# Kernel tuning notes

Measured on AMD Instinct MI355X. Metric: run time of the kernel, lower is better.

The kernel has to match this reference:

```python
import jax, jax.numpy as jnp
import numpy as np

B, S, D, L, H = 2, 2048, 2048, 3, 16
DH = D // H
BLOCK = 16
NA = 64
Q = NA * BLOCK
KV = S + Q
VOCAB = 32000
MASK_ID = 31999
GAMMA = 7.0
EPS = 1e-6


def _rope(x, pos):
    # x: [B,H,T,DH], pos: [B,T]
    half = DH // 2
    inv = 1.0 / (10000.0 ** (jnp.arange(half, dtype=jnp.float32) / half))
    ang = pos[:, None, :, None].astype(jnp.float32) * inv  # [B,1,T,half]
    c, s = jnp.cos(ang), jnp.sin(ang)
    x1, x2 = x[..., :half], x[..., half:]
    return jnp.concatenate([x1 * c - x2 * s, x2 * c + x1 * s], axis=-1)


def setup_inputs() -> dict:
    key = jax.random.key(0)
    ks = jax.random.split(key, 12)
    w = lambda k, shp: 0.02 * jax.random.normal(k, shp, jnp.float32)
    return {
        'input_ids': jax.random.randint(ks[0], (B, S), 0, VOCAB, dtype=jnp.int32),
        'hidden_states': jax.random.normal(ks[1], (L, B, S, D), jnp.float32),
        'loss_mask': jnp.ones((B, S), jnp.int32),
        'lm_head_weight': w(ks[2], (VOCAB, D)),
        'norm_weight': jnp.ones((D,), jnp.float32),
        'anchor_positions': jnp.sort(jax.random.randint(ks[3], (B, NA), 0, S - BLOCK, dtype=jnp.int32), axis=-1),
        'ctx_proj_w': w(ks[4], (D, L * D)),
        'embed_table': w(ks[5], (VOCAB, D)),
        'wq': w(ks[6], (D, D)),
        'wk': w(ks[7], (D, D)),
        'wv': w(ks[8], (D, D)),
        'wo': w(ks[9], (D, D)),
    }


def reference(input_ids, hidden_states, loss_mask, lm_head_weight, norm_weight,
              anchor_positions, ctx_proj_w, embed_table, wq, wk, wv, wo):
    # --- context feature: concat L target-layer hiddens, project to D ---
    ctx_cat = jnp.transpose(hidden_states, (1, 2, 0, 3)).reshape(B, S, L * D)
    ctx = jnp.einsum('bsf,df->bsd', ctx_cat, ctx_proj_w)

    # --- position ids (context: 0..S-1; draft block i starts at anchor_i) ---
    ctx_pos = jnp.broadcast_to(jnp.arange(S, dtype=jnp.int32), (B, S))
    draft_pos = (anchor_positions[:, :, None] + jnp.arange(BLOCK, dtype=jnp.int32)[None, None, :]).reshape(B, Q)

    # --- draft input (anchor token + MASKs) and labels ---
    off = jnp.arange(Q, dtype=jnp.int32) % BLOCK                       # [Q]
    anchor_per_tok = jnp.repeat(anchor_positions, BLOCK, axis=1)       # [B,Q]
    anchor_tok = jnp.take_along_axis(input_ids, anchor_positions, axis=1)
    draft_ids = jnp.where(off[None, :] == 0, jnp.repeat(anchor_tok, BLOCK, axis=1), MASK_ID)
    labels = jnp.where(off[None, :] == 0, -100,
                       jnp.take_along_axis(input_ids, anchor_per_tok + off[None, :], axis=1))

    # --- block-causal mask: [B,Q,KV] ---
    qi = jnp.arange(Q, dtype=jnp.int32)
    ki = jnp.arange(KV, dtype=jnp.int32)
    qb = qi // BLOCK                                                   # [Q]
    apos = anchor_positions[:, qb]                                     # [B,Q]
    ctx_vis = (ki[None, None, :] < S) & (ki[None, None, :] < apos[:, :, None])
    kb = (ki - S) // BLOCK
    draft_vis = (ki >= S)[None, :] & (qb[:, None] == kb[None, :])      # [Q,KV]
    mask = ctx_vis | draft_vis[None]                                   # [B,Q,KV]

    # --- single RoPE attention layer: draft queries over [context; draft] ---
    emb = embed_table[draft_ids]                                       # [B,Q,D]
    x_kv = jnp.concatenate([ctx, emb], axis=1)                         # [B,KV,D]
    pos_kv = jnp.concatenate([ctx_pos, draft_pos], axis=1)             # [B,KV]
    q = _rope((emb @ wq.T).reshape(B, Q, H, DH).transpose(0, 2, 1, 3), draft_pos)
    k = _rope((x_kv @ wk.T).reshape(B, KV, H, DH).transpose(0, 2, 1, 3), pos_kv)
    v = (x_kv @ wv.T).reshape(B, KV, H, DH).transpose(0, 2, 1, 3)
    scores = jnp.einsum('bhqd,bhkd->bhqk', q, k) / np.float32(np.sqrt(DH))
    scores = jnp.where(mask[:, None], scores, jnp.float32(-1e30))
    attn = jax.nn.softmax(scores, axis=-1)
    out = jnp.einsum('bhqk,bhkd->bhqd', attn, v).transpose(0, 2, 1, 3).reshape(B, Q, D) @ wo.T
    hidden = emb + out

    # --- RMSNorm + LM head ---
    hidden = hidden * jax.lax.rsqrt(jnp.mean(hidden * hidden, -1, keepdims=True) + EPS) * norm_weight
    logits = hidden @ lm_head_weight.T                                 # [B,Q,VOCAB]

    # --- decay-weighted CE loss + accuracy ---
    logp = jax.nn.log_softmax(logits, axis=-1)
    lab = jnp.where(labels < 0, 0, labels)
    nll = -jnp.take_along_axis(logp, lab[..., None], axis=-1)[..., 0]
    valid = labels != -100
    offf = off.astype(jnp.float32)
    decay = jnp.where(off == 0, 0.0, jnp.exp(-(offf - 1.0) / GAMMA))   # [Q]
    w = decay[None, :] * valid.astype(jnp.float32)
    loss = jnp.sum(nll * w) / jnp.maximum(jnp.sum(w), 1e-6)
    preds = jnp.argmax(logits, axis=-1).astype(labels.dtype)
    acc = jnp.sum((preds == labels) & valid) / jnp.maximum(jnp.sum(valid), 1)
    return loss, acc.astype(jnp.float32)
```

## Files before the change

kernel.cpp:

```cpp
#include <hip/hip_runtime.h>

#define B_ 2
#define S_ 2048
#define D_ 2048
#define L_ 3
#define H_ 16
#define DH_ 128
#define BLK_ 16
#define NA_ 64
#define Q_ 1024
#define KV_ 3072
#define VOCAB_ 32000
#define MASK_ID_ 31999
#define NTOK_ (B_*Q_)
#define VT2_ (VOCAB_/256)
#define NCHUNK_ 4

typedef __attribute__((ext_vector_type(8))) short bf16x8;
typedef __attribute__((ext_vector_type(4))) float f32x4;
typedef const __attribute__((address_space(1))) void* gptr_t;
typedef __attribute__((address_space(3))) void* lptr_t;

__device__ inline unsigned short f2bf(float x) {
  unsigned int u = __float_as_uint(x);
  unsigned int r = (u + 0x7fff + ((u >> 16) & 1)) >> 16;
  return (unsigned short)r;
}
__device__ inline float bf2f(unsigned short u) {
  return __uint_as_float(((unsigned int)u) << 16);
}

__global__ void k_meta(const int* __restrict__ ids, const int* __restrict__ anchors,
                       int* __restrict__ dids, int* __restrict__ dpos, int* __restrict__ labels) {
  int t = blockIdx.x * 256 + threadIdx.x;
  if (t >= NTOK_) return;
  int b = t >> 10, qi = t & 1023;
  int a = qi >> 4, off = qi & 15;
  int ap = anchors[b * NA_ + a];
  dpos[t] = ap + off;
  dids[t] = (off == 0) ? ids[b * S_ + ap] : MASK_ID_;
  labels[t] = (off == 0) ? -100 : ids[b * S_ + ap + off];
}

__global__ void k_cvt(const float* __restrict__ in, unsigned short* __restrict__ out, int n4) {
  int i = blockIdx.x * 256 + threadIdx.x;
  if (i >= n4) return;
  float4 v = ((const float4*)in)[i];
  ushort4 o;
  o.x = f2bf(v.x); o.y = f2bf(v.y); o.z = f2bf(v.z); o.w = f2bf(v.w);
  ((ushort4*)out)[i] = o;
}

__global__ void k_cvt_ctx(const float* __restrict__ hs, unsigned short* __restrict__ out) {
  int bi = blockIdx.x;
  int l = bi % 3, row = bi / 3;
  const float4* src = (const float4*)(hs + ((size_t)l * B_ * S_ + row) * (size_t)D_);
  ushort4* dst = (ushort4*)(out + (size_t)row * (3 * D_) + (size_t)l * D_);
  for (int i = threadIdx.x; i < D_ / 4; i += 256) {
    float4 v = src[i];
    ushort4 o;
    o.x = f2bf(v.x); o.y = f2bf(v.y); o.z = f2bf(v.z); o.w = f2bf(v.w);
    dst[i] = o;
  }
}

__global__ void k_gather(const float* __restrict__ table, const int* __restrict__ dids,
                         unsigned short* __restrict__ x_kv) {
  int row = blockIdx.x;
  int b = row >> 10, qi = row & 1023;
  const float4* src = (const float4*)(table + (size_t)dids[row] * D_);
  ushort4* dst = (ushort4*)(x_kv + ((size_t)b * KV_ + S_ + qi) * D_);
  for (int i = threadIdx.x; i < D_ / 4; i += 256) {
    float4 v = src[i];
    ushort4 o;
    o.x = f2bf(v.x); o.y = f2bf(v.y); o.z = f2bf(v.z); o.w = f2bf(v.w);
    dst[i] = o;
  }
}

#define STAGE3(s_, kt_)                                                        \
  {                                                                            \
    unsigned short* as_ = &Asl[s_][0];                                         \
    unsigned short* bs_ = &Bsl[s_][0];                                         \
    _Pragma("unroll")                                                          \
    for (int i_ = 0; i_ < 2; ++i_)                                             \
      __builtin_amdgcn_global_load_lds((gptr_t)(A + aoff[i_] + (kt_)),         \
          (lptr_t)((char*)as_ + adst[i_]), 16, 0, 0);                          \
    _Pragma("unroll")                                                          \
    for (int i_ = 0; i_ < 4; ++i_)                                             \
      __builtin_amdgcn_global_load_lds((gptr_t)(Bw + boff[i_] + (kt_)),        \
          (lptr_t)((char*)bs_ + bdst[i_]), 16, 0, 0);                          \
  }

template <int CMODE>
__global__ __launch_bounds__(512, 1) void k_gemm3(
    const unsigned short* __restrict__ A, const unsigned short* __restrict__ Bw,
    float* __restrict__ Cf, unsigned short* __restrict__ Cb,
    int M, int N, int K, int adivlog, long long abump, int cdivlog, long long cbump,
    const int* __restrict__ labels, float* __restrict__ pm, float* __restrict__ ps,
    int* __restrict__ pbi, float* __restrict__ plab) {
  __shared__ unsigned short Asl[3][128 * 64];
  __shared__ unsigned short Bsl[3][256 * 64];
  int ntm = M >> 7;
  int per = gridDim.x >> 3;
  int wgid = (blockIdx.x & 7) * per + (blockIdx.x >> 3);
  int by = wgid % ntm, bx = wgid / ntm;
  int rowbase = by << 7, colbase = bx << 8;
  int tid = threadIdx.x, l = tid & 63, w = tid >> 6;
  int wm = w >> 2, wn = w & 3;
  int lo = l & 15, hi = l >> 4;

  long long aoff[2]; int adst[2];
#pragma unroll
  for (int i = 0; i < 2; ++i) {
    int rl = w * 16 + i * 8 + (l >> 3);
    int cu = (l & 7) ^ (rl & 7);
    long long ra = rowbase + rl;
    aoff[i] = ra * K + (ra >> adivlog) * abump + cu * 8;
    adst[i] = (w * 128 + i * 64) * 16;
  }
  long long boff[4]; int bdst[4];
#pragma unroll
  for (int i = 0; i < 4; ++i) {
    int rl = w * 32 + i * 8 + (l >> 3);
    int cu = (l & 7) ^ (rl & 7);
    long long rb = colbase + rl;
    boff[i] = rb * K + cu * 8;
    bdst[i] = (w * 256 + i * 64) * 16;
  }
  int ard[4][2], brd[4][2];
#pragma unroll
  for (int m = 0; m < 4; ++m)
#pragma unroll
    for (int ks = 0; ks < 2; ++ks) {
      int row = wm * 64 + m * 16 + lo;
      int pos = ((ks << 2) | hi) ^ (row & 7);
      ard[m][ks] = row * 64 + pos * 8;
      row = wn * 64 + m * 16 + lo;
      pos = ((ks << 2) | hi) ^ (row & 7);
      brd[m][ks] = row * 64 + pos * 8;
    }

  f32x4 acc[4][4];
#pragma unroll
  for (int m = 0; m < 4; ++m)
#pragma unroll
    for (int n = 0; n < 4; ++n) acc[m][n] = (f32x4){0.f, 0.f, 0.f, 0.f};

  int NT = K >> 6;
  STAGE3(0, 0);
  STAGE3(1, 64);
  STAGE3(2, 128);

  int s = 0;
  for (int t = 0; t < NT; ++t) {
    if (t < NT - 2)       asm volatile("s_waitcnt vmcnt(12)" ::: "memory");
    else if (t == NT - 2) asm volatile("s_waitcnt vmcnt(6)" ::: "memory");
    else                  asm volatile("s_waitcnt vmcnt(0)" ::: "memory");
    __builtin_amdgcn_s_barrier();
    asm volatile("" ::: "memory");
    const unsigned short* as_ = &Asl[s][0];
    const unsigned short* bs_ = &Bsl[s][0];
    bf16x8 af[4][2], bg[4][2];
#pragma unroll
    for (int m = 0; m < 4; ++m)
#pragma unroll
      for (int ks = 0; ks < 2; ++ks) {
        af[m][ks] = *(const bf16x8*)(as_ + ard[m][ks]);
        bg[m][ks] = *(const bf16x8*)(bs_ + brd[m][ks]);
      }
    __builtin_amdgcn_s_setprio(1);
#pragma unroll
    for (int m = 0; m < 4; ++m)
#pragma unroll
      for (int n = 0; n < 4; ++n) {
        acc[m][n] = __builtin_amdgcn_mfma_f32_16x16x32_bf16(af[m][0], bg[n][0], acc[m][n], 0, 0, 0);
        acc[m][n] = __builtin_amdgcn_mfma_f32_16x16x32_bf16(af[m][1], bg[n][1], acc[m][n], 0, 0, 0);
      }
    __builtin_amdgcn_s_setprio(0);
    __builtin_amdgcn_sched_barrier(0);
    asm volatile("" ::: "memory");
    __builtin_amdgcn_s_barrier();
    if (t + 3 < NT) STAGE3(s, (t + 3) << 6);
    s = (s == 2) ? 0 : s + 1;
  }

  if (CMODE == 0 || CMODE == 1) {
#pragma unroll
    for (int m = 0; m < 4; ++m)
#pragma unroll
      for (int n = 0; n < 4; ++n)
#pragma unroll
        for (int r4 = 0; r4 < 4; ++r4) {
          int row = rowbase + wm * 64 + m * 16 + hi * 4 + r4;
          int col = colbase + wn * 64 + n * 16 + lo;
          size_t addr = (size_t)row * N + (size_t)(row >> cdivlog) * cbump + col;
          if (CMODE == 0) Cf[addr] = acc[m][n][r4];
          else Cb[addr] = f2bf(acc[m][n][r4]);
        }
  } else {
    float* f = (float*)&Asl[0][0];
    int* ii = (int*)&Bsl[0][0];
    if (tid < 128) { f[1152 + tid] = -3.0e38f; ii[640 + tid] = labels[rowbase + tid]; }
    __syncthreads();
#pragma unroll
    for (int m = 0; m < 4; ++m)
#pragma unroll
      for (int r4 = 0; r4 < 4; ++r4) {
        int rl = wm * 64 + m * 16 + hi * 4 + r4;
        float mx = acc[m][0][r4];
        int arg = colbase + wn * 64 + lo;
#pragma unroll
        for (int n = 1; n < 4; ++n) {
          float v = acc[m][n][r4];
          int c = colbase + wn * 64 + n * 16 + lo;
          if (v > mx) { mx = v; arg = c; }
        }
#pragma unroll
        for (int d = 1; d < 16; d <<= 1) {
          float om = __shfl_xor(mx, d);
          int oc = __shfl_xor(arg, d);
          if (om > mx || (om == mx && oc < arg)) { mx = om; arg = oc; }
        }
        if (lo == 0) { f[wn * 128 + rl] = mx; ii[wn * 128 + rl] = arg; }
      }
    __syncthreads();
    if (tid < 128) {
      float m0 = f[tid]; int a0 = ii[tid];
#pragma unroll
      for (int x = 1; x < 4; ++x) {
        float v = f[x * 128 + tid]; int c = ii[x * 128 + tid];
        if (v > m0 || (v == m0 && c < a0)) { m0 = v; a0 = c; }
      }
      f[1024 + tid] = m0; ii[512 + tid] = a0;
    }
    __syncthreads();
#pragma unroll
    for (int m = 0; m < 4; ++m)
#pragma unroll
      for (int r4 = 0; r4 < 4; ++r4) {
        int rl = wm * 64 + m * 16 + hi * 4 + r4;
        float gm = f[1024 + rl];
        float sacc = 0.f;
#pragma unroll
        for (int n = 0; n < 4; ++n) sacc += __expf(acc[m][n][r4] - gm);
#pragma unroll
        for (int d = 1; d < 16; d <<= 1) sacc += __shfl_xor(sacc, d);
        if (lo == 0) f[512 + wn * 128 + rl] = sacc;
        int lab = ii[640 + rl];
        int rel = lab - colbase;
        if (rel >= 0 && rel < 256 && (rel >> 6) == wn && (rel & 15) == lo) {
          int n_own = (rel >> 4) & 3;
#pragma unroll
          for (int n = 0; n < 4; ++n)
            if (n == n_own) f[1152 + rl] = acc[m][n][r4];
        }
      }
    __syncthreads();
    if (tid < 128) {
      int grow = rowbase + tid;
      size_t p = (size_t)grow * VT2_ + bx;
      pm[p] = f[1024 + tid];
      ps[p] = f[512 + tid] + f[512 + 128 + tid] + f[512 + 256 + tid] + f[512 + 384 + tid];
      pbi[p] = ii[512 + tid];
      plab[p] = f[1152 + tid];
    }
  }
}

template <int CMODE, int MAP>
__global__ __launch_bounds__(256) void k_mfma_bt(
    const unsigned short* __restrict__ A, const unsigned short* __restrict__ Bw,
    float* __restrict__ Cf, unsigned short* __restrict__ Cb,
    int M, int N, int K, int adivlog, long long abump, int cdivlog, long long cbump) {
  __shared__ unsigned short As[128 * 32];
  __shared__ unsigned short Bs[128 * 32];
  int ntn = N >> 7;
  int bx = blockIdx.x % ntn, by = blockIdx.x / ntn;
  int rowbase = by << 7, colbase = bx << 7;
  int tid = threadIdx.x, lane = tid & 63, w = tid >> 6;
  int wr = w >> 1, wc = w & 1;
  int lo = lane & 15, hi = lane >> 4;

  f32x4 acc[4][4];
#pragma unroll
  for (int m = 0; m < 4; ++m)
#pragma unroll
    for (int n = 0; n < 4; ++n) acc[m][n] = (f32x4){0.f, 0.f, 0.f, 0.f};

  for (int kt = 0; kt < K; kt += 32) {
#pragma unroll
    for (int i = 0; i < 2; ++i) {
      int seg = i * 4 + w;
      int rloc = seg * 16 + (lane >> 2);
      int kcol = kt + ((lane & 3) << 3);
      int ra = rowbase + rloc;
      long long aoff = (long long)ra * K + (long long)(ra >> adivlog) * abump + kcol;
      __builtin_amdgcn_global_load_lds((gptr_t)(A + aoff), (lptr_t)(As + seg * 512), 16, 0, 0);
      int rb = colbase + rloc;
      long long boff = (long long)rb * K + kcol;
      __builtin_amdgcn_global_load_lds((gptr_t)(Bw + boff), (lptr_t)(Bs + seg * 512), 16, 0, 0);
    }
    __syncthreads();
    bf16x8 af[4], bfv[4];
#pragma unroll
    for (int m = 0; m < 4; ++m) {
      int row = wr * 64 + m * 16 + lo;
      af[m] = *(const bf16x8*)(As + row * 32 + (hi << 3));
    }
#pragma unroll
    for (int n = 0; n < 4; ++n) {
      int row = wc * 64 + n * 16 + lo;
      bfv[n] = *(const bf16x8*)(Bs + row * 32 + (hi << 3));
    }
#pragma unroll
    for (int m = 0; m < 4; ++m)
#pragma unroll
      for (int n = 0; n < 4; ++n)
        acc[m][n] = __builtin_amdgcn_mfma_f32_16x16x32_bf16(af[m], bfv[n], acc[m][n], 0, 0, 0);
    __syncthreads();
  }
#pragma unroll
  for (int m = 0; m < 4; ++m)
#pragma unroll
    for (int n = 0; n < 4; ++n)
#pragma unroll
      for (int r4 = 0; r4 < 4; ++r4) {
        int row = rowbase + wr * 64 + m * 16 + hi * 4 + r4;
        int col = colbase + wc * 64 + n * 16 + lo;
        int bb = row >= KV_;
        int kv = row - bb * KV_;
        size_t addr = ((size_t)(bb * H_ + (col >> 7)) * 128 + (col & 127)) * KV_ + kv;
        Cb[addr] = f2bf(acc[m][n][r4]);
      }
}

__global__ void k_rope(unsigned short* __restrict__ x, const int* __restrict__ dpos, int mode) {
  int idx = blockIdx.x * 256 + threadIdx.x;
  int j = idx & 63;
  int h = (idx >> 6) & 15;
  int row = idx >> 10;
  int pos;
  if (mode == 0) {
    if (row >= NTOK_) return;
    pos = dpos[row];
  } else {
    if (row >= B_ * KV_) return;
    int b = row / KV_, kvi = row % KV_;
    pos = (kvi < S_) ? kvi : dpos[b * Q_ + (kvi - S_)];
  }
  float inv = expf(-(float)j * (9.210340371976184f / 64.f));
  float ang = (float)pos * inv;
  float c = cosf(ang), s = sinf(ang);
  unsigned short* p = x + (size_t)row * D_ + h * DH_ + j;
  float x1 = bf2f(p[0]), x2 = bf2f(p[64]);
  p[0] = f2bf(x1 * c - x2 * s);
  p[64] = f2bf(x2 * c + x1 * s);
}

__global__ __launch_bounds__(256) void k_attn_part(
    const unsigned short* __restrict__ qb, const unsigned short* __restrict__ kb,
    const unsigned short* __restrict__ vt, const int* __restrict__ anchors,
    float* __restrict__ pm_att, float* __restrict__ pl_att, float* __restrict__ po_att) {
  __shared__ __align__(16) unsigned short P_all[4][16 * 40];
  int w = threadIdx.x >> 6, lane = threadIdx.x & 63;
  int blk = blockIdx.x * 4 + w;
  int chunk = blk & 3, h = (blk >> 2) & 15, a = (blk >> 6) & 63, b = blk >> 12;
  int ql = lane & 15, p = lane >> 4;
  int apos = anchors[b * NA_ + a];

  int cstart = chunk << 9;
  int cend = min(apos, cstart + 512);
  int len = (cend > cstart) ? (cend - cstart) : 0;
  int ntile = (len + 31) >> 5;
  int total = ntile + ((chunk == 3) ? 1 : 0);

  if (total == 0) {
    if (p == 0) { pm_att[blk * 16 + ql] = -3.0e38f; pl_att[blk * 16 + ql] = 0.f; }
    return;
  }
  unsigned short* P = P_all[w];

  const unsigned short* qbase = qb + ((size_t)(b * Q_ + a * 16 + ql)) * D_ + h * DH_;
  bf16x8 qf[4];
#pragma unroll
  for (int ks = 0; ks < 4; ++ks)
    qf[ks] = *(const bf16x8*)(qbase + ks * 32 + p * 8);

  const unsigned short* kbb = kb + (size_t)b * KV_ * D_ + h * DH_;
  const unsigned short* vtb = vt + ((size_t)(b * H_ + h)) * 128 * KV_;

  f32x4 o[8];
#pragma unroll
  for (int nt = 0; nt < 8; ++nt) o[nt] = (f32x4){0.f, 0.f, 0.f, 0.f};
  float mrun = -3.0e38f, lrun = 0.f;
  const float scl = 0.08838834764831845f;

  for (int t = 0; t < total; ++t) {
    bool isdraft = (chunk == 3) && (t == ntile);
    int ktb = isdraft ? (S_ + a * 16) : (cstart + (t << 5));
    int vc = isdraft ? 16 : min(32, cend - ktb);
    float s[2][4];
#pragma unroll
    for (int g = 0; g < 2; ++g) {
      if (g * 16 < vc) {
        f32x4 accs = (f32x4){0.f, 0.f, 0.f, 0.f};
        const unsigned short* krow = kbb + (size_t)(ktb + g * 16 + ql) * D_;
#pragma unroll
        for (int ks = 0; ks < 4; ++ks) {
          bf16x8 kf = *(const bf16x8*)(krow + ks * 32 + p * 8);
          accs = __builtin_amdgcn_mfma_f32_16x16x32_bf16(kf, qf[ks], accs, 0, 0, 0);
        }
#pragma unroll
        for (int r = 0; r < 4; ++r) {
          int kl = g * 16 + p * 4 + r;
          s[g][r] = (kl < vc) ? accs[r] * scl : -3.0e38f;
        }
      } else {
#pragma unroll
        for (int r = 0; r < 4; ++r) s[g][r] = -3.0e38f;
      }
    }
    float mt = s[0][0];
#pragma unroll
    for (int g = 0; g < 2; ++g)
#pragma unroll
      for (int r = 0; r < 4; ++r) mt = fmaxf(mt, s[g][r]);
    mt = fmaxf(mt, __shfl_xor(mt, 16));
    mt = fmaxf(mt, __shfl_xor(mt, 32));
    float mnew = fmaxf(mrun, mt);
    float corr = __expf(mrun - mnew);
    float psum = 0.f;
#pragma unroll
    for (int g = 0; g < 2; ++g) {
      float p0 = __expf(s[g][0] - mnew), p1 = __expf(s[g][1] - mnew);
      float p2 = __expf(s[g][2] - mnew), p3 = __expf(s[g][3] - mnew);
      psum += p0 + p1 + p2 + p3;
      ushort2 w0, w1;
      w0.x = f2bf(p0); w0.y = f2bf(p1); w1.x = f2bf(p2); w1.y = f2bf(p3);
      int eo = ql * 40 + g * 16 + p * 4;
      *(ushort2*)(P + eo) = w0;
      *(ushort2*)(P + eo + 2) = w1;
    }
    psum += __shfl_xor(psum, 16);
    psum += __shfl_xor(psum, 32);
    lrun = lrun * corr + psum;
    mrun = mnew;
    float cr[4];
#pragma unroll
    for (int r = 0; r < 4; ++r) cr[r] = __shfl(corr, p * 4 + r);
#pragma unroll
    for (int nt = 0; nt < 8; ++nt)
#pragma unroll
      for (int r = 0; r < 4; ++r) o[nt][r] *= cr[r];
    bf16x8 pf = *(const bf16x8*)(P + ql * 40 + p * 8);
#pragma unroll
    for (int nt = 0; nt < 8; ++nt) {
      bf16x8 vf = *(const bf16x8*)(vtb + (size_t)(nt * 16 + ql) * KV_ + ktb + p * 8);
      o[nt] = __builtin_amdgcn_mfma_f32_16x16x32_bf16(pf, vf, o[nt], 0, 0, 0);
    }
  }
  if (p == 0) { pm_att[blk * 16 + ql] = mrun; pl_att[blk * 16 + ql] = lrun; }
  float* pob = po_att + (size_t)blk * 2048;
#pragma unroll
  for (int nt = 0; nt < 8; ++nt)
#pragma unroll
    for (int r = 0; r < 4; ++r)
      pob[(p * 4 + r) * 128 + nt * 16 + ql] = o[nt][r];
}

__global__ __launch_bounds__(256) void k_attn_combine(
    const float* __restrict__ pm_att, const float* __restrict__ pl_att,
    const float* __restrict__ po_att, unsigned short* __restrict__ ob) {
  int base = blockIdx.x;
  int h = base & 15, a = (base >> 4) & 63, b = base >> 10;
  int d = threadIdx.x & 127, qh = threadIdx.x >> 7;
  int pbase = base * 4;
#pragma unroll
  for (int qq = 0; qq < 8; ++qq) {
    int q = qh * 8 + qq;
    float m0 = pm_att[(pbase + 0) * 16 + q], m1 = pm_att[(pbase + 1) * 16 + q];
    float m2 = pm_att[(pbase + 2) * 16 + q], m3 = pm_att[(pbase + 3) * 16 + q];
    float mg = fmaxf(fmaxf(m0, m1), fmaxf(m2, m3));
    float w0 = __expf(m0 - mg), w1 = __expf(m1 - mg);
    float w2 = __expf(m2 - mg), w3 = __expf(m3 - mg);
    float lg = pl_att[(pbase + 0) * 16 + q] * w0 + pl_att[(pbase + 1) * 16 + q] * w1 +
               pl_att[(pbase + 2) * 16 + q] * w2 + pl_att[(pbase + 3) * 16 + q] * w3;
    float od = po_att[(size_t)(pbase + 0) * 2048 + q * 128 + d] * w0 +
               po_att[(size_t)(pbase + 1) * 2048 + q * 128 + d] * w1 +
               po_att[(size_t)(pbase + 2) * 2048 + q * 128 + d] * w2 +
               po_att[(size_t)(pbase + 3) * 2048 + q * 128 + d] * w3;
    ob[((size_t)(b * Q_ + a * 16 + q)) * D_ + h * DH_ + d] = f2bf(od / lg);
  }
}

__global__ void k_rmsnorm(const unsigned short* __restrict__ x_kv, const float* __restrict__ proj,
                          const float* __restrict__ nw, unsigned short* __restrict__ outp) {
  int row = blockIdx.x;
  int b = row >> 10, qi = row & 1023;
  const unsigned short* emb = x_kv + ((size_t)b * KV_ + S_ + qi) * D_;
  const float* pr = proj + (size_t)row * D_;
  __shared__ float red[256];
  float h[8];
  float ssum = 0.f;
#pragma unroll
  for (int i = 0; i < 8; ++i) {
    int d = threadIdx.x + i * 256;
    h[i] = bf2f(emb[d]) + pr[d];
    ssum += h[i] * h[i];
  }
  red[threadIdx.x] = ssum;
  __syncthreads();
  for (int s = 128; s; s >>= 1) {
    if (threadIdx.x < s) red[threadIdx.x] += red[threadIdx.x + s];
    __syncthreads();
  }
  float scale = rsqrtf(red[0] / (float)D_ + 1e-6f);
#pragma unroll
  for (int i = 0; i < 8; ++i) {
    int d = threadIdx.x + i * 256;
    outp[(size_t)row * D_ + d] = f2bf(h[i] * scale * nw[d]);
  }
}

__global__ void k_combine(const float* __restrict__ pm, const float* __restrict__ ps,
                          const int* __restrict__ pbi, const float* __restrict__ plab,
                          const int* __restrict__ labels, float* __restrict__ ts) {
  int t = blockIdx.x * 256 + threadIdx.x;
  if (t >= NTOK_) return;
  const float* pmr = pm + (size_t)t * VT2_;
  const float* psr = ps + (size_t)t * VT2_;
  const int* pbir = pbi + (size_t)t * VT2_;
  const float* plabr = plab + (size_t)t * VT2_;
  float M = -3.0e38f; int bi = 0;
  for (int x = 0; x < VT2_; ++x) {
    float v = pmr[x];
    if (v > M) { M = v; bi = pbir[x]; }
  }
  float ssum = 0.f, labl = -3.0e38f;
  for (int x = 0; x < VT2_; ++x) {
    ssum += psr[x] * __expf(pmr[x] - M);
    labl = fmaxf(labl, plabr[x]);
  }
  float lse = M + logf(ssum);
  int lab = labels[t];
  int off = t & 15;
  float valid = (lab != -100) ? 1.f : 0.f;
  float w = (off == 0) ? 0.f : __expf(-(float)(off - 1) / 7.0f);
  w *= valid;
  float nll = (lab != -100) ? (lse - labl) : 0.f;
  float correct = (valid > 0.f && bi == lab) ? 1.f : 0.f;
  ts[t * 4 + 0] = nll * w;
  ts[t * 4 + 1] = w;
  ts[t * 4 + 2] = correct;
  ts[t * 4 + 3] = valid;
}

__global__ void k_finalize(const float* __restrict__ ts, float* __restrict__ out) {
  __shared__ float r0[256], r1[256], r2[256], r3[256];
  int tid = threadIdx.x;
  float s0 = 0, s1 = 0, s2 = 0, s3 = 0;
  for (int t = tid; t < NTOK_; t += 256) {
    s0 += ts[t * 4 + 0]; s1 += ts[t * 4 + 1];
    s2 += ts[t * 4 + 2]; s3 += ts[t * 4 + 3];
  }
  r0[tid] = s0; r1[tid] = s1; r2[tid] = s2; r3[tid] = s3;
  __syncthreads();
  for (int s = 128; s; s >>= 1) {
    if (tid < s) {
      r0[tid] += r0[tid + s]; r1[tid] += r1[tid + s];
      r2[tid] += r2[tid + s]; r3[tid] += r3[tid + s];
    }
    __syncthreads();
  }
  if (tid == 0) {
    out[0] = r0[0] / fmaxf(r1[0], 1e-6f);
    out[1] = r2[0] / fmaxf(r3[0], 1.f);
  }
}

extern "C" void kernel_launch(void* const* d_in, const int* in_sizes, int n_in,
                              void* d_out, int out_size, void* d_ws, size_t ws_size,
                              hipStream_t stream) {
  const int* input_ids = (const int*)d_in[0];
  const float* hs = (const float*)d_in[1];
  const float* lm_head = (const float*)d_in[3];
  const float* norm_w = (const float*)d_in[4];
  const int* anchors = (const int*)d_in[5];
  const float* ctx_w = (const float*)d_in[6];
  const float* embed = (const float*)d_in[7];
  const float* wq = (const float*)d_in[8];
  const float* wk = (const float*)d_in[9];
  const float* wv = (const float*)d_in[10];
  const float* wo = (const float*)d_in[11];
  float* out = (float*)d_out;

  char* base = (char*)d_ws;
  size_t off = 0;
  unsigned short* x_kv_bf = (unsigned short*)(base + off); off += (size_t)B_ * KV_ * D_ * 2;
  unsigned short* wkb = (unsigned short*)(base + off); off += (size_t)D_ * D_ * 2;
  unsigned short* wvb = (unsigned short*)(base + off); off += (size_t)D_ * D_ * 2;
  unsigned short* wqb = (unsigned short*)(base + off); off += (size_t)D_ * D_ * 2;
  unsigned short* wob = (unsigned short*)(base + off); off += (size_t)D_ * D_ * 2;
  unsigned short* hidden_bf = (unsigned short*)(base + off); off += (size_t)NTOK_ * D_ * 2;
  unsigned short* attn_bf = (unsigned short*)(base + off); off += (size_t)NTOK_ * D_ * 2;
  float* proj = (float*)(base + off); off += (size_t)NTOK_ * D_ * 4;
  float* pm = (float*)(base + off); off += (size_t)NTOK_ * 250 * 4;
  float* psum = (float*)(base + off); off += (size_t)NTOK_ * 250 * 4;
  float* plab = (float*)(base + off); off += (size_t)NTOK_ * 250 * 4;
  int* pbi = (int*)(base + off); off += (size_t)NTOK_ * 250 * 4;
  float* tstats = (float*)(base + off); off += (size_t)NTOK_ * 4 * 4;
  int* dids = (int*)(base + off); off += NTOK_ * 4;
  int* dpos = (int*)(base + off); off += NTOK_ * 4;
  int* labels = (int*)(base + off); off += NTOK_ * 4;
  char* regA = base + off;
  const size_t SLACK = 65536;
  unsigned short* ctxA = (unsigned short*)(regA);
  unsigned short* ctx_wbf = (unsigned short*)(regA + 50331648);
  unsigned short* kbuf = (unsigned short*)(regA + 50331648 + 25165824);
  unsigned short* vtbuf = (unsigned short*)(regA + 50331648 + 2 * 25165824 + SLACK);
  unsigned short* qbuf = (unsigned short*)(regA + 50331648 + 3 * 25165824 + 2 * SLACK);
  unsigned short* lm_bf = (unsigned short*)(regA);
  float* po_att = (float*)(regA);
  float* pm_att = (float*)(regA + 67108864);
  float* pl_att = (float*)(regA + 67108864 + 524288);

  k_meta<<<(NTOK_ + 255) / 256, 256, 0, stream>>>(input_ids, anchors, dids, dpos, labels);
  k_cvt<<<((D_ * (L_ * D_) / 4) + 255) / 256, 256, 0, stream>>>(ctx_w, ctx_wbf, D_ * (L_ * D_) / 4);
  k_cvt<<<((D_ * D_ / 4) + 255) / 256, 256, 0, stream>>>(wk, wkb, D_ * D_ / 4);
  k_cvt<<<((D_ * D_ / 4) + 255) / 256, 256, 0, stream>>>(wv, wvb, D_ * D_ / 4);
  k_cvt<<<((D_ * D_ / 4) + 255) / 256, 256, 0, stream>>>(wq, wqb, D_ * D_ / 4);
  k_cvt<<<((D_ * D_ / 4) + 255) / 256, 256, 0, stream>>>(wo, wob, D_ * D_ / 4);
  k_cvt_ctx<<<B_ * S_ * L_, 256, 0, stream>>>(hs, ctxA);
  k_gather<<<NTOK_, 256, 0, stream>>>(embed, dids, x_kv_bf);

  k_gemm3<1><<<(4096 / 128) * (2048 / 256), 512, 0, stream>>>(
      ctxA, ctx_wbf, nullptr, x_kv_bf, 4096, 2048, 6144, 30, 0LL, 11, (long long)Q_ * D_,
      nullptr, nullptr, nullptr, nullptr, nullptr);
  k_gemm3<1><<<(6144 / 128) * (2048 / 256), 512, 0, stream>>>(
      x_kv_bf, wkb, nullptr, kbuf, 6144, 2048, 2048, 30, 0LL, 30, 0LL,
      nullptr, nullptr, nullptr, nullptr, nullptr);
  k_mfma_bt<3, 0><<<(6144 / 128) * (2048 / 128), 256, 0, stream>>>(
      x_kv_bf, wvb, nullptr, vtbuf, 6144, 2048, 2048, 30, 0LL, 30, 0LL);
  k_gemm3<1><<<(2048 / 128) * (2048 / 256), 512, 0, stream>>>(
      x_kv_bf + (size_t)S_ * D_, wqb, nullptr, qbuf, 2048, 2048, 2048, 10,
      (long long)(KV_ - Q_) * D_, 30, 0LL,
      nullptr, nullptr, nullptr, nullptr, nullptr);
  k_rope<<<(NTOK_ * H_ * 64) / 256, 256, 0, stream>>>(qbuf, dpos, 0);
  k_rope<<<(B_ * KV_ * H_ * 64) / 256, 256, 0, stream>>>(kbuf, dpos, 1);
  k_attn_part<<<(B_ * NA_ * H_ * NCHUNK_) / 4, 256, 0, stream>>>(
      qbuf, kbuf, vtbuf, anchors, pm_att, pl_att, po_att);
  k_attn_combine<<<B_ * NA_ * H_, 256, 0, stream>>>(pm_att, pl_att, po_att, attn_bf);
  k_gemm3<0><<<(2048 / 128) * (2048 / 256), 512, 0, stream>>>(
      attn_bf, wob, proj, nullptr, 2048, 2048, 2048, 30, 0LL, 30, 0LL,
      nullptr, nullptr, nullptr, nullptr, nullptr);
  k_rmsnorm<<<NTOK_, 256, 0, stream>>>(x_kv_bf, proj, norm_w, hidden_bf);
  k_cvt<<<((VOCAB_ * D_ / 4) + 255) / 256, 256, 0, stream>>>(lm_head, lm_bf, VOCAB_ * D_ / 4);
  k_gemm3<2><<<(2048 / 128) * (VOCAB_ / 256), 512, 0, stream>>>(
      hidden_bf, lm_bf, nullptr, nullptr, 2048, VOCAB_, 2048, 30, 0LL, 30, 0LL,
      labels, pm, psum, pbi, plab);
  k_combine<<<(NTOK_ + 255) / 256, 256, 0, stream>>>(pm, psum, pbi, plab, labels, tstats);
  k_finalize<<<1, 256, 0, stream>>>(tstats, out);
}
```

Baseline: 1.346 ms.

## Replace triple-buffered GEMMs with 256x256 double-buffered LM-head GEMM and simpler projections

The LM-head GEMM with the fused CE/argmax epilogue now uses a 256x256 tile with two-stage LDS buffering instead of a 128x256 triple-buffered tile. Each warp computes 8x4 MFMA tiles, which raises reuse of the B fragments. The context, K, Q and O projection GEMMs move from the triple-buffered 512-thread kernel to the generic 256-thread 128x128 kernel, which gains a plain row-major store epilogue. The larger tile cuts global traffic on the dominant vocab GEMM but raises register pressure and leaves only one prefetch stage to hide latency. The projection GEMMs may lose throughput from the simpler kernel.

```diff
diff --git a/kernel.cpp b/kernel.cpp
--- a/kernel.cpp
+++ b/kernel.cpp
@@ -78,197 +78,174 @@
   }
 }
 
-#define STAGE3(s_, kt_)                                                        \
+#define STAGE2(buf_, kt_)                                                      \
   {                                                                            \
-    unsigned short* as_ = &Asl[s_][0];                                         \
-    unsigned short* bs_ = &Bsl[s_][0];                                         \
     _Pragma("unroll")                                                          \
-    for (int i_ = 0; i_ < 2; ++i_)                                             \
+    for (int i_ = 0; i_ < 4; ++i_) {                                           \
       __builtin_amdgcn_global_load_lds((gptr_t)(A + aoff[i_] + (kt_)),         \
-          (lptr_t)((char*)as_ + adst[i_]), 16, 0, 0);                          \
-    _Pragma("unroll")                                                          \
-    for (int i_ = 0; i_ < 4; ++i_)                                             \
+          (lptr_t)((char*)Asl2 + (buf_) * 32768 + abase[i_]), 16, 0, 0);       \
       __builtin_amdgcn_global_load_lds((gptr_t)(Bw + boff[i_] + (kt_)),        \
-          (lptr_t)((char*)bs_ + bdst[i_]), 16, 0, 0);                          \
-  }
-
-template <int CMODE>
-__global__ __launch_bounds__(512, 1) void k_gemm3(
+          (lptr_t)((char*)Bsl2 + (buf_) * 32768 + bbase[i_]), 16, 0, 0);       \
+    }                                                                          \
+  }
+
+__global__ __launch_bounds__(512, 1) void k_gemm2(
     const unsigned short* __restrict__ A, const unsigned short* __restrict__ Bw,
-    float* __restrict__ Cf, unsigned short* __restrict__ Cb,
-    int M, int N, int K, int adivlog, long long abump, int cdivlog, long long cbump,
+    int M, int N, int K,
     const int* __restrict__ labels, float* __restrict__ pm, float* __restrict__ ps,
     int* __restrict__ pbi, float* __restrict__ plab) {
-  __shared__ unsigned short Asl[3][128 * 64];
-  __shared__ unsigned short Bsl[3][256 * 64];
-  int ntm = M >> 7;
+  __shared__ unsigned short Asl2[2 * 256 * 64];
+  __shared__ unsigned short Bsl2[2 * 256 * 64];
+  int ntm = M >> 8;
   int per = gridDim.x >> 3;
   int wgid = (blockIdx.x & 7) * per + (blockIdx.x >> 3);
   int by = wgid % ntm, bx = wgid / ntm;
-  int rowbase = by << 7, colbase = bx << 8;
+  int rowbase = by << 8, colbase = bx << 8;
   int tid = threadIdx.x, l = tid & 63, w = tid >> 6;
   int wm = w >> 2, wn = w & 3;
   int lo = l & 15, hi = l >> 4;
 
-  long long aoff[2]; int adst[2];
-#pragma unroll
-  for (int i = 0; i < 2; ++i) {
-    int rl = w * 16 + i * 8 + (l >> 3);
-    int cu = (l & 7) ^ (rl & 7);
-    long long ra = rowbase + rl;
-    aoff[i] = ra * K + (ra >> adivlog) * abump + cu * 8;
-    adst[i] = (w * 128 + i * 64) * 16;
-  }
-  long long boff[4]; int bdst[4];
+  long long aoff[4], boff[4];
+  int abase[4], bbase[4];
 #pragma unroll
   for (int i = 0; i < 4; ++i) {
-    int rl = w * 32 + i * 8 + (l >> 3);
-    int cu = (l & 7) ^ (rl & 7);
-    long long rb = colbase + rl;
-    boff[i] = rb * K + cu * 8;
-    bdst[i] = (w * 256 + i * 64) * 16;
-  }
-  int ard[4][2], brd[4][2];
-#pragma unroll
-  for (int m = 0; m < 4; ++m)
+    int rb8 = (w * 4 + i) * 8;
+    int r = rb8 + (l >> 3);
+    int cu = (l & 7) ^ (r & 7);
+    aoff[i] = (long long)(rowbase + r) * K + cu * 8;
+    boff[i] = (long long)(colbase + r) * K + cu * 8;
+    abase[i] = rb8 * 128;
+    bbase[i] = rb8 * 128;
+  }
+  int ard[8][2], brd[4][2];
+#pragma unroll
+  for (int m = 0; m < 8; ++m)
 #pragma unroll
     for (int ks = 0; ks < 2; ++ks) {
-      int row = wm * 64 + m * 16 + lo;
-      int pos = ((ks << 2) | hi) ^ (row & 7);
-      ard[m][ks] = row * 64 + pos * 8;
-      row = wn * 64 + m * 16 + lo;
-      pos = ((ks << 2) | hi) ^ (row & 7);
-      brd[m][ks] = row * 64 + pos * 8;
-    }
-
-  f32x4 acc[4][4];
-#pragma unroll
-  for (int m = 0; m < 4; ++m)
+      int r = wm * 128 + m * 16 + lo;
+      int p = ((ks << 2) | hi) ^ (r & 7);
+      ard[m][ks] = r * 64 + p * 8;
+    }
+#pragma unroll
+  for (int n = 0; n < 4; ++n)
+#pragma unroll
+    for (int ks = 0; ks < 2; ++ks) {
+      int r = wn * 64 + n * 16 + lo;
+      int p = ((ks << 2) | hi) ^ (r & 7);
+      brd[n][ks] = r * 64 + p * 8;
+    }
+
+  f32x4 acc[8][4];
+#pragma unroll
+  for (int m = 0; m < 8; ++m)
 #pragma unroll
     for (int n = 0; n < 4; ++n) acc[m][n] = (f32x4){0.f, 0.f, 0.f, 0.f};
 
   int NT = K >> 6;
-  STAGE3(0, 0);
-  STAGE3(1, 64);
-  STAGE3(2, 128);
-
-  int s = 0;
+  int cur = 0;
+  STAGE2(0, 0);
   for (int t = 0; t < NT; ++t) {
-    if (t < NT - 2)       asm volatile("s_waitcnt vmcnt(12)" ::: "memory");
-    else if (t == NT - 2) asm volatile("s_waitcnt vmcnt(6)" ::: "memory");
-    else                  asm volatile("s_waitcnt vmcnt(0)" ::: "memory");
+    if (t + 1 < NT) {
+      STAGE2(cur ^ 1, (t + 1) << 6);
+      asm volatile("s_waitcnt vmcnt(8)" ::: "memory");
+    } else {
+      asm volatile("s_waitcnt vmcnt(0)" ::: "memory");
+    }
     __builtin_amdgcn_s_barrier();
     asm volatile("" ::: "memory");
-    const unsigned short* as_ = &Asl[s][0];
-    const unsigned short* bs_ = &Bsl[s][0];
-    bf16x8 af[4][2], bg[4][2];
-#pragma unroll
-    for (int m = 0; m < 4; ++m)
-#pragma unroll
-      for (int ks = 0; ks < 2; ++ks) {
-        af[m][ks] = *(const bf16x8*)(as_ + ard[m][ks]);
-        bg[m][ks] = *(const bf16x8*)(bs_ + brd[m][ks]);
-      }
+    const unsigned short* as_ = Asl2 + cur * 16384;
+    const unsigned short* bs_ = Bsl2 + cur * 16384;
     __builtin_amdgcn_s_setprio(1);
 #pragma unroll
-    for (int m = 0; m < 4; ++m)
-#pragma unroll
-      for (int n = 0; n < 4; ++n) {
-        acc[m][n] = __builtin_amdgcn_mfma_f32_16x16x32_bf16(af[m][0], bg[n][0], acc[m][n], 0, 0, 0);
-        acc[m][n] = __builtin_amdgcn_mfma_f32_16x16x32_bf16(af[m][1], bg[n][1], acc[m][n], 0, 0, 0);
-      }
+    for (int ks = 0; ks < 2; ++ks) {
+      bf16x8 af[8], bg[4];
+#pragma unroll
+      for (int m = 0; m < 8; ++m) af[m] = *(const bf16x8*)(as_ + ard[m][ks]);
+#pragma unroll
+      for (int n = 0; n < 4; ++n) bg[n] = *(const bf16x8*)(bs_ + brd[n][ks]);
+#pragma unroll
+      for (int m = 0; m < 8; ++m)
+#pragma unroll
+        for (int n = 0; n < 4; ++n)
+          acc[m][n] = __builtin_amdgcn_mfma_f32_16x16x32_bf16(af[m], bg[n], acc[m][n], 0, 0, 0);
+    }
     __builtin_amdgcn_s_setprio(0);
     __builtin_amdgcn_sched_barrier(0);
     asm volatile("" ::: "memory");
     __builtin_amdgcn_s_barrier();
-    if (t + 3 < NT) STAGE3(s, (t + 3) << 6);
-    s = (s == 2) ? 0 : s + 1;
-  }
-
-  if (CMODE == 0 || CMODE == 1) {
-#pragma unroll
-    for (int m = 0; m < 4; ++m)
-#pragma unroll
-      for (int n = 0; n < 4; ++n)
-#pragma unroll
-        for (int r4 = 0; r4 < 4; ++r4) {
-          int row = rowbase + wm * 64 + m * 16 + hi * 4 + r4;
-          int col = colbase + wn * 64 + n * 16 + lo;
-          size_t addr = (size_t)row * N + (size_t)(row >> cdivlog) * cbump + col;
-          if (CMODE == 0) Cf[addr] = acc[m][n][r4];
-          else Cb[addr] = f2bf(acc[m][n][r4]);
-        }
-  } else {
-    float* f = (float*)&Asl[0][0];
-    int* ii = (int*)&Bsl[0][0];
-    if (tid < 128) { f[1152 + tid] = -3.0e38f; ii[640 + tid] = labels[rowbase + tid]; }
-    __syncthreads();
-#pragma unroll
-    for (int m = 0; m < 4; ++m)
-#pragma unroll
-      for (int r4 = 0; r4 < 4; ++r4) {
-        int rl = wm * 64 + m * 16 + hi * 4 + r4;
-        float mx = acc[m][0][r4];
-        int arg = colbase + wn * 64 + lo;
-#pragma unroll
-        for (int n = 1; n < 4; ++n) {
-          float v = acc[m][n][r4];
-          int c = colbase + wn * 64 + n * 16 + lo;
-          if (v > mx) { mx = v; arg = c; }
-        }
-#pragma unroll
-        for (int d = 1; d < 16; d <<= 1) {
-          float om = __shfl_xor(mx, d);
-          int oc = __shfl_xor(arg, d);
-          if (om > mx || (om == mx && oc < arg)) { mx = om; arg = oc; }
-        }
-        if (lo == 0) { f[wn * 128 + rl] = mx; ii[wn * 128 + rl] = arg; }
+    cur ^= 1;
+  }
+
+  float* f = (float*)Asl2;
+  int* ii = (int*)Bsl2;
+  __syncthreads();
+  if (tid < 256) { f[2304 + tid] = -3.0e38f; ii[1280 + tid] = labels[rowbase + tid]; }
+  __syncthreads();
+#pragma unroll
+  for (int m = 0; m < 8; ++m)
+#pragma unroll
+    for (int r4 = 0; r4 < 4; ++r4) {
+      int rl = wm * 128 + m * 16 + hi * 4 + r4;
+      float mx = acc[m][0][r4];
+      int arg = colbase + wn * 64 + lo;
+#pragma unroll
+      for (int n = 1; n < 4; ++n) {
+        float v = acc[m][n][r4];
+        int c = colbase + wn * 64 + n * 16 + lo;
+        if (v > mx) { mx = v; arg = c; }
       }
-    __syncthreads();
-    if (tid < 128) {
-      float m0 = f[tid]; int a0 = ii[tid];
-#pragma unroll
-      for (int x = 1; x < 4; ++x) {
-        float v = f[x * 128 + tid]; int c = ii[x * 128 + tid];
-        if (v > m0 || (v == m0 && c < a0)) { m0 = v; a0 = c; }
+#pragma unroll
+      for (int d = 1; d < 16; d <<= 1) {
+        float om = __shfl_xor(mx, d);
+        int oc = __shfl_xor(arg, d);
+        if (om > mx || (om == mx && oc < arg)) { mx = om; arg = oc; }
       }
-      f[1024 + tid] = m0; ii[512 + tid] = a0;
-    }
-    __syncthreads();
-#pragma unroll
-    for (int m = 0; m < 4; ++m)
-#pragma unroll
-      for (int r4 = 0; r4 < 4; ++r4) {
-        int rl = wm * 64 + m * 16 + hi * 4 + r4;
-        float gm = f[1024 + rl];
-        float sacc = 0.f;
-#pragma unroll
-        for (int n = 0; n < 4; ++n) sacc += __expf(acc[m][n][r4] - gm);
-#pragma unroll
-        for (int d = 1; d < 16; d <<= 1) sacc += __shfl_xor(sacc, d);
-        if (lo == 0) f[512 + wn * 128 + rl] = sacc;
-        int lab = ii[640 + rl];
-        int rel = lab - colbase;
-        if (rel >= 0 && rel < 256 && (rel >> 6) == wn && (rel & 15) == lo) {
-          int n_own = (rel >> 4) & 3;
-#pragma unroll
-          for (int n = 0; n < 4; ++n)
-            if (n == n_own) f[1152 + rl] = acc[m][n][r4];
-        }
+      if (lo == 0) { f[wn * 256 + rl] = mx; ii[wn * 256 + rl] = arg; }
+    }
+  __syncthreads();
+  if (tid < 256) {
+    float m0 = f[tid]; int a0 = ii[tid];
+#pragma unroll
+    for (int x = 1; x < 4; ++x) {
+      float v = f[x * 256 + tid]; int c = ii[x * 256 + tid];
+      if (v > m0 || (v == m0 && c < a0)) { m0 = v; a0 = c; }
+    }
+    f[2048 + tid] = m0; ii[1024 + tid] = a0;
+  }
+  __syncthreads();
+#pragma unroll
+  for (int m = 0; m < 8; ++m)
+#pragma unroll
+    for (int r4 = 0; r4 < 4; ++r4) {
+      int rl = wm * 128 + m * 16 + hi * 4 + r4;
+      float gm = f[2048 + rl];
+      float sacc = 0.f;
+#pragma unroll
+      for (int n = 0; n < 4; ++n) sacc += __expf(acc[m][n][r4] - gm);
+#pragma unroll
+      for (int d = 1; d < 16; d <<= 1) sacc += __shfl_xor(sacc, d);
+      if (lo == 0) f[1024 + wn * 256 + rl] = sacc;
+      int lab = ii[1280 + rl];
+      int rel = lab - colbase;
+      if (rel >= 0 && rel < 256 && (rel >> 6) == wn && (rel & 15) == lo) {
+        int n_own = (rel >> 4) & 3;
+#pragma unroll
+        for (int n = 0; n < 4; ++n)
+          if (n == n_own) f[2304 + rl] = acc[m][n][r4];
       }
-    __syncthreads();
-    if (tid < 128) {
-      int grow = rowbase + tid;
-      size_t p = (size_t)grow * VT2_ + bx;
-      pm[p] = f[1024 + tid];
-      ps[p] = f[512 + tid] + f[512 + 128 + tid] + f[512 + 256 + tid] + f[512 + 384 + tid];
-      pbi[p] = ii[512 + tid];
-      plab[p] = f[1152 + tid];
-    }
-  }
-}
-
-template <int CMODE, int MAP>
+    }
+  __syncthreads();
+  if (tid < 256) {
+    int grow = rowbase + tid;
+    size_t p = (size_t)grow * VT2_ + bx;
+    pm[p] = f[2048 + tid];
+    ps[p] = f[1024 + tid] + f[1024 + 256 + tid] + f[1024 + 512 + tid] + f[1024 + 768 + tid];
+    pbi[p] = ii[1024 + tid];
+    plab[p] = f[2304 + tid];
+  }
+}
+
+template <int CMODE>
 __global__ __launch_bounds__(256) void k_mfma_bt(
     const unsigned short* __restrict__ A, const unsigned short* __restrict__ Bw,
     float* __restrict__ Cf, unsigned short* __restrict__ Cb,
@@ -320,19 +297,35 @@
         acc[m][n] = __builtin_amdgcn_mfma_f32_16x16x32_bf16(af[m], bfv[n], acc[m][n], 0, 0, 0);
     __syncthreads();
   }
-#pragma unroll
-  for (int m = 0; m < 4; ++m)
-#pragma unroll
-    for (int n = 0; n < 4; ++n)
-#pragma unroll
-      for (int r4 = 0; r4 < 4; ++r4) {
-        int row = rowbase + wr * 64 + m * 16 + hi * 4 + r4;
-        int col = colbase + wc * 64 + n * 16 + lo;
-        int bb = row >= KV_;
-        int kv = row - bb * KV_;
-        size_t addr = ((size_t)(bb * H_ + (col >> 7)) * 128 + (col & 127)) * KV_ + kv;
-        Cb[addr] = f2bf(acc[m][n][r4]);
-      }
+
+  if (CMODE == 0 || CMODE == 1) {
+#pragma unroll
+    for (int m = 0; m < 4; ++m)
+#pragma unroll
+      for (int n = 0; n < 4; ++n)
+#pragma unroll
+        for (int r4 = 0; r4 < 4; ++r4) {
+          int row = rowbase + wr * 64 + m * 16 + hi * 4 + r4;
+          int col = colbase + wc * 64 + n * 16 + lo;
+          size_t addr = (size_t)row * N + (size_t)(row >> cdivlog) * cbump + col;
+          if (CMODE == 0) Cf[addr] = acc[m][n][r4];
+          else Cb[addr] = f2bf(acc[m][n][r4]);
+        }
+  } else {
+#pragma unroll
+    for (int m = 0; m < 4; ++m)
+#pragma unroll
+      for (int n = 0; n < 4; ++n)
+#pragma unroll
+        for (int r4 = 0; r4 < 4; ++r4) {
+          int row = rowbase + wr * 64 + m * 16 + hi * 4 + r4;
+          int col = colbase + wc * 64 + n * 16 + lo;
+          int bb = row >= KV_;
+          int kv = row - bb * KV_;
+          size_t addr = ((size_t)(bb * H_ + (col >> 7)) * 128 + (col & 127)) * KV_ + kv;
+          Cb[addr] = f2bf(acc[m][n][r4]);
+        }
+  }
 }
 
 __global__ void k_rope(unsigned short* __restrict__ x, const int* __restrict__ dpos, int mode) {
@@ -605,10 +598,10 @@
   unsigned short* hidden_bf = (unsigned short*)(base + off); off += (size_t)NTOK_ * D_ * 2;
   unsigned short* attn_bf = (unsigned short*)(base + off); off += (size_t)NTOK_ * D_ * 2;
   float* proj = (float*)(base + off); off += (size_t)NTOK_ * D_ * 4;
-  float* pm = (float*)(base + off); off += (size_t)NTOK_ * 250 * 4;
-  float* psum = (float*)(base + off); off += (size_t)NTOK_ * 250 * 4;
-  float* plab = (float*)(base + off); off += (size_t)NTOK_ * 250 * 4;
-  int* pbi = (int*)(base + off); off += (size_t)NTOK_ * 250 * 4;
+  float* pm = (float*)(base + off); off += (size_t)NTOK_ * VT2_ * 4;
+  float* psum = (float*)(base + off); off += (size_t)NTOK_ * VT2_ * 4;
+  float* plab = (float*)(base + off); off += (size_t)NTOK_ * VT2_ * 4;
+  int* pbi = (int*)(base + off); off += (size_t)NTOK_ * VT2_ * 4;
   float* tstats = (float*)(base + off); off += (size_t)NTOK_ * 4 * 4;
   int* dids = (int*)(base + off); off += NTOK_ * 4;
   int* dpos = (int*)(base + off); off += NTOK_ * 4;
@@ -634,31 +627,26 @@
   k_cvt_ctx<<<B_ * S_ * L_, 256, 0, stream>>>(hs, ctxA);
   k_gather<<<NTOK_, 256, 0, stream>>>(embed, dids, x_kv_bf);
 
-  k_gemm3<1><<<(4096 / 128) * (2048 / 256), 512, 0, stream>>>(
-      ctxA, ctx_wbf, nullptr, x_kv_bf, 4096, 2048, 6144, 30, 0LL, 11, (long long)Q_ * D_,
-      nullptr, nullptr, nullptr, nullptr, nullptr);
-  k_gemm3<1><<<(6144 / 128) * (2048 / 256), 512, 0, stream>>>(
-      x_kv_bf, wkb, nullptr, kbuf, 6144, 2048, 2048, 30, 0LL, 30, 0LL,
-      nullptr, nullptr, nullptr, nullptr, nullptr);
-  k_mfma_bt<3, 0><<<(6144 / 128) * (2048 / 128), 256, 0, stream>>>(
+  k_mfma_bt<1><<<(4096 / 128) * (2048 / 128), 256, 0, stream>>>(
+      ctxA, ctx_wbf, nullptr, x_kv_bf, 4096, 2048, 6144, 30, 0LL, 11, (long long)Q_ * D_);
+  k_mfma_bt<1><<<(6144 / 128) * (2048 / 128), 256, 0, stream>>>(
+      x_kv_bf, wkb, nullptr, kbuf, 6144, 2048, 2048, 30, 0LL, 30, 0LL);
+  k_mfma_bt<3><<<(6144 / 128) * (2048 / 128), 256, 0, stream>>>(
       x_kv_bf, wvb, nullptr, vtbuf, 6144, 2048, 2048, 30, 0LL, 30, 0LL);
-  k_gemm3<1><<<(2048 / 128) * (2048 / 256), 512, 0, stream>>>(
+  k_mfma_bt<1><<<(2048 / 128) * (2048 / 128), 256, 0, stream>>>(
       x_kv_bf + (size_t)S_ * D_, wqb, nullptr, qbuf, 2048, 2048, 2048, 10,
-      (long long)(KV_ - Q_) * D_, 30, 0LL,
-      nullptr, nullptr, nullptr, nullptr, nullptr);
+      (long long)(KV_ - Q_) * D_, 30, 0LL);
   k_rope<<<(NTOK_ * H_ * 64) / 256, 256, 0, stream>>>(qbuf, dpos, 0);
   k_rope<<<(B_ * KV_ * H_ * 64) / 256, 256, 0, stream>>>(kbuf, dpos, 1);
   k_attn_part<<<(B_ * NA_ * H_ * NCHUNK_) / 4, 256, 0, stream>>>(
       qbuf, kbuf, vtbuf, anchors, pm_att, pl_att, po_att);
   k_attn_combine<<<B_ * NA_ * H_, 256, 0, stream>>>(pm_att, pl_att, po_att, attn_bf);
-  k_gemm3<0><<<(2048 / 128) * (2048 / 256), 512, 0, stream>>>(
-      attn_bf, wob, proj, nullptr, 2048, 2048, 2048, 30, 0LL, 30, 0LL,
-      nullptr, nullptr, nullptr, nullptr, nullptr);
+  k_mfma_bt<0><<<(2048 / 128) * (2048 / 128), 256, 0, stream>>>(
+      attn_bf, wob, proj, nullptr, 2048, 2048, 2048, 30, 0LL, 30, 0LL);
   k_rmsnorm<<<NTOK_, 256, 0, stream>>>(x_kv_bf, proj, norm_w, hidden_bf);
   k_cvt<<<((VOCAB_ * D_ / 4) + 255) / 256, 256, 0, stream>>>(lm_head, lm_bf, VOCAB_ * D_ / 4);
-  k_gemm3<2><<<(2048 / 128) * (VOCAB_ / 256), 512, 0, stream>>>(
-      hidden_bf, lm_bf, nullptr, nullptr, 2048, VOCAB_, 2048, 30, 0LL, 30, 0LL,
-      labels, pm, psum, pbi, plab);
+  k_gemm2<<<(2048 / 256) * (VOCAB_ / 256), 512, 0, stream>>>(
+      hidden_bf, lm_bf, 2048, VOCAB_, 2048, labels, pm, psum, pbi, plab);
   k_combine<<<(NTOK_ + 255) / 256, 256, 0, stream>>>(pm, psum, pbi, plab, labels, tstats);
   k_finalize<<<1, 256, 0, stream>>>(tstats, out);
 }
```

Measured after the change: 1.211 ms, median of 3. -10.0%, faster.
